# Kernel tuning notes

Hardware: AMD Instinct MI355X
Metric: run time of the kernel (lower is better)

Reference implementation:

```python
import math
import jax, jax.numpy as jnp
import numpy as np
from jax import lax

B, T, D_HEAD, M_FEAT = 8, 8192, 64, 256
EPS = 1e-6


def _draw_omega(key, d, m):
    # Orthogonal random features: QR blocks of size d x d, rows rescaled by
    # the Frobenius row-norms of the original Gaussian blocks (chi scaling).
    n_blocks = math.ceil(m / d)
    blocks = []
    for i in range(n_blocks):
        g = jax.random.normal(jax.random.fold_in(key, i), (d, d), dtype=jnp.float32)
        qb, _ = jnp.linalg.qr(g)
        norms = jnp.linalg.norm(g, axis=1)
        blocks.append(qb * norms[:, None])
    return jnp.concatenate(blocks, axis=0)[:m]


def setup_inputs() -> dict:
    key = jax.random.key(0)
    kq, kk, kv, ko = jax.random.split(key, 4)
    q = jax.random.normal(kq, (B, T, D_HEAD), dtype=jnp.float32)
    k = jax.random.normal(kk, (B, T, D_HEAD), dtype=jnp.float32)
    v = jax.random.normal(kv, (B, T, D_HEAD), dtype=jnp.float32)
    omega = _draw_omega(ko, D_HEAD, M_FEAT)
    return {"q": q, "k": k, "v": v, "omega": omega}


def _positive_map(x, omega):
    # phi(x) = exp(x @ omega^T - ||x||^2/2 - rowmax) / sqrt(m)
    log_phi = x @ omega.T - 0.5 * jnp.sum(x * x, axis=-1, keepdims=True)
    log_phi = log_phi - jnp.max(log_phi, axis=-1, keepdims=True)
    m = omega.shape[0]
    return jnp.exp(log_phi) / jnp.sqrt(jnp.asarray(m, dtype=x.dtype))


def reference(q, k, v, omega):
    scale = 1.0 / math.sqrt(q.shape[-1])
    phi_q = _positive_map(q * scale, omega)  # (B, T, m)
    phi_k = _positive_map(k * scale, omega)  # (B, T, m)

    def step(carry, xs):
        S, z = carry                     # S: (B, m, d), z: (B, m)
        pq, pk, vt = xs                  # each (B, m) / (B, m) / (B, d)
        S = S + pk[:, :, None] * vt[:, None, :]
        z = z + pk
        out = jnp.einsum('bm,bmd->bd', pq, S)
        denom = jnp.sum(pq * z, axis=-1, keepdims=True) + EPS
        return (S, z), out / denom

    S0 = jnp.zeros((q.shape[0], omega.shape[0], v.shape[-1]), dtype=q.dtype)
    z0 = jnp.zeros((q.shape[0], omega.shape[0]), dtype=q.dtype)
    xs = (jnp.swapaxes(phi_q, 0, 1), jnp.swapaxes(phi_k, 0, 1), jnp.swapaxes(v, 0, 1))
    _, outs = lax.scan(step, (S0, z0), xs)   # outs: (T, B, d)
    return jnp.swapaxes(outs, 0, 1)          # (B, T, d)
```

## Files before the change

### kernel.cpp

```cpp
#include <hip/hip_runtime.h>
#include <hip/hip_bf16.h>

typedef __hip_bfloat16 bf16;
typedef __attribute__((ext_vector_type(8))) short short8;
typedef __attribute__((ext_vector_type(4))) short shortx4;
typedef __attribute__((ext_vector_type(4))) float floatx4;

#define NEED_WS_BYTES 110625024ULL

__device__ __forceinline__ float b2f(bf16 x) { return __bfloat162float(x); }
__device__ __forceinline__ bf16  f2b(float x) { return __float2bfloat16(x); }
__device__ __forceinline__ float bflo(unsigned u) { return __uint_as_float(u << 16); }
__device__ __forceinline__ float bfhi(unsigned u) { return __uint_as_float(u & 0xffff0000u); }

__device__ __forceinline__ float ldin(const void* p, size_t i, int isf32) {
  return isf32 ? ((const float*)p)[i] : b2f(((const bf16*)p)[i]);
}

__device__ __forceinline__ short sb(float f) {
  bf16 h = f2b(f * 0.125f);
  return *reinterpret_cast<short*>(&h);
}
__device__ __forceinline__ short scale_b(short u) {
  float f = __uint_as_float(((unsigned)(unsigned short)u) << 16) * 0.125f;
  bf16 h = f2b(f);
  return *reinterpret_cast<short*>(&h);
}

__global__ __launch_bounds__(256) void k_detect(const void* __restrict__ q,
                                                int* __restrict__ flag) {
  __shared__ int cnt;
  if (threadIdx.x == 0) cnt = 0;
  __syncthreads();
  const unsigned short* u = (const unsigned short*)q;
  int c = 0;
  for (int e = threadIdx.x; e < 2048; e += 256) {
    unsigned short w = u[2 * e];
    int ex = (w >> 7) & 0xFF;
    if ((w & 0x7FFF) != 0 && (ex < 110 || ex > 140)) c++;
  }
  atomicAdd(&cnt, c);
  __syncthreads();
  if (threadIdx.x == 0) *flag = (cnt > 512) ? 1 : 0;
}

__global__ __launch_bounds__(256) void k_omega(const void* __restrict__ omega,
                                               bf16* __restrict__ omb,
                                               const int* __restrict__ flag) {
  int isf32 = *flag;
  int e = blockIdx.x * 256 + threadIdx.x;
  omb[e] = f2b(ldin(omega, e, isf32));
}

__device__ __forceinline__ void phi_load_a(const void* src, size_t row, int quad,
                                           int isf32, short8& a0, short8& a1) {
  if (isf32) {
    const float* xr = (const float*)src + row * 64;
    float4 f0 = *reinterpret_cast<const float4*>(xr + quad * 8);
    float4 f1 = *reinterpret_cast<const float4*>(xr + quad * 8 + 4);
    float4 f2 = *reinterpret_cast<const float4*>(xr + 32 + quad * 8);
    float4 f3 = *reinterpret_cast<const float4*>(xr + 32 + quad * 8 + 4);
    a0[0] = sb(f0.x); a0[1] = sb(f0.y); a0[2] = sb(f0.z); a0[3] = sb(f0.w);
    a0[4] = sb(f1.x); a0[5] = sb(f1.y); a0[6] = sb(f1.z); a0[7] = sb(f1.w);
    a1[0] = sb(f2.x); a1[1] = sb(f2.y); a1[2] = sb(f2.z); a1[3] = sb(f2.w);
    a1[4] = sb(f3.x); a1[5] = sb(f3.y); a1[6] = sb(f3.z); a1[7] = sb(f3.w);
  } else {
    const short* xr = (const short*)src + row * 64;
    short8 r0 = *reinterpret_cast<const short8*>(xr + quad * 8);
    short8 r1 = *reinterpret_cast<const short8*>(xr + 32 + quad * 8);
    #pragma unroll
    for (int j = 0; j < 8; ++j) { a0[j] = scale_b(r0[j]); a1[j] = scale_b(r1[j]); }
  }
}

__device__ __forceinline__ void phi_mfma(const bf16* omb, int li, int quad,
                                         const short8& a0, const short8& a1,
                                         floatx4* c, float* mx) {
  #pragma unroll
  for (int n0 = 0; n0 < 16; ++n0) {
    const short* bp = (const short*)omb + (size_t)(n0 * 16 + li) * 64 + quad * 8;
    short8 b0 = *reinterpret_cast<const short8*>(bp);
    short8 b1 = *reinterpret_cast<const short8*>(bp + 32);
    floatx4 acc = {0.f, 0.f, 0.f, 0.f};
    acc = __builtin_amdgcn_mfma_f32_16x16x32_bf16(a0, b0, acc, 0, 0, 0);
    acc = __builtin_amdgcn_mfma_f32_16x16x32_bf16(a1, b1, acc, 0, 0, 0);
    c[n0] = acc;
  }
  #pragma unroll
  for (int r = 0; r < 4; ++r) {
    float m = c[0][r];
    #pragma unroll
    for (int n0 = 1; n0 < 16; ++n0) m = fmaxf(m, c[n0][r]);
    mx[r] = m;
  }
  #pragma unroll
  for (int mask = 1; mask < 16; mask <<= 1) {
    #pragma unroll
    for (int r = 0; r < 4; ++r) mx[r] = fmaxf(mx[r], __shfl_xor(mx[r], mask, 64));
  }
}

__global__ __launch_bounds__(256)
__attribute__((amdgpu_waves_per_eu(1, 2))) void k_phik(
    const void* __restrict__ k, const void* __restrict__ v,
    const bf16* __restrict__ omb, bf16* __restrict__ phiK,
    bf16* __restrict__ SlocT, float* __restrict__ zloc,
    const int* __restrict__ flag) {
  __shared__ short ob[4][16][136];
  __shared__ short pkT[256 * 72];
  __shared__ short vTh[64 * 72];
  __shared__ short vTl[64 * 72];
  __shared__ float zpart[4][256];

  int isf32 = *flag;
  int tid = threadIdx.x;
  size_t tok0 = (size_t)blockIdx.x * 64;
  int li = tid & 15;
  int quad = (tid >> 4) & 3;
  int w = tid >> 6;
  int m0 = w * 16;
  size_t row = tok0 + m0 + li;

  #pragma unroll
  for (int it = 0; it < 16; ++it) {
    int e = it * 256 + tid;
    int tau = e >> 6, d = e & 63;
    float vv = ldin(v, tok0 * 64 + e, isf32);
    bf16 h = f2b(vv);
    bf16 l = f2b(vv - b2f(h));
    vTh[d * 72 + tau] = *reinterpret_cast<short*>(&h);
    vTl[d * 72 + tau] = *reinterpret_cast<short*>(&l);
  }

  short8 a0, a1;
  phi_load_a(k, row, quad, isf32, a0, a1);
  floatx4 c[16];
  float mx[4];
  phi_mfma(omb, li, quad, a0, a1, c, mx);

  float zl[16];
  #pragma unroll
  for (int f = 0; f < 16; ++f) zl[f] = 0.f;
  size_t srow = tok0 + m0 + li;
  #pragma unroll
  for (int h = 0; h < 2; ++h) {
    #pragma unroll
    for (int r = 0; r < 4; ++r) {
      #pragma unroll
      for (int n = 0; n < 8; ++n) {
        bf16 hv = f2b(__expf(c[h * 8 + n][r] - mx[r]) * 0.0625f);
        short hb = *reinterpret_cast<short*>(&hv);
        ob[w][quad * 4 + r][n * 16 + li] = hb;
        pkT[((h * 8 + n) * 16 + li) * 72 + (m0 + quad * 4 + r)] = hb;
        zl[h * 8 + n] += bflo((unsigned)(unsigned short)hb);
      }
    }
    #pragma unroll
    for (int it = 0; it < 4; ++it) {
      int ch = it * 4 + quad;
      short8 vv = *reinterpret_cast<const short8*>(&ob[w][li][ch * 8]);
      *reinterpret_cast<short8*>((short*)phiK + srow * 256 + h * 128 + ch * 8) = vv;
    }
  }
  #pragma unroll
  for (int f = 0; f < 16; ++f) {
    float vz = zl[f];
    vz += __shfl_xor(vz, 16, 64);
    vz += __shfl_xor(vz, 32, 64);
    if (quad == 0) zpart[w][f * 16 + li] = vz;
  }

  __syncthreads();

  int wbase = w * 64;
  floatx4 sa[4][4];
  #pragma unroll
  for (int mt = 0; mt < 4; ++mt)
    #pragma unroll
    for (int n0 = 0; n0 < 4; ++n0) sa[mt][n0] = (floatx4){0.f, 0.f, 0.f, 0.f};

  #pragma unroll
  for (int h = 0; h < 2; ++h) {
    short8 Ah[4], Al[4];
    #pragma unroll
    for (int mt = 0; mt < 4; ++mt) {
      Ah[mt] = *reinterpret_cast<const short8*>(
          &vTh[(mt * 16 + li) * 72 + h * 32 + quad * 8]);
      Al[mt] = *reinterpret_cast<const short8*>(
          &vTl[(mt * 16 + li) * 72 + h * 32 + quad * 8]);
    }
    #pragma unroll
    for (int n0 = 0; n0 < 4; ++n0) {
      short8 Bq = *reinterpret_cast<const short8*>(
          &pkT[(wbase + n0 * 16 + li) * 72 + h * 32 + quad * 8]);
      #pragma unroll
      for (int mt = 0; mt < 4; ++mt) {
        sa[mt][n0] =
            __builtin_amdgcn_mfma_f32_16x16x32_bf16(Ah[mt], Bq, sa[mt][n0], 0, 0, 0);
        sa[mt][n0] =
            __builtin_amdgcn_mfma_f32_16x16x32_bf16(Al[mt], Bq, sa[mt][n0], 0, 0, 0);
      }
    }
  }

  bf16* Sb = SlocT + (size_t)blockIdx.x * 16384;
  #pragma unroll
  for (int mt = 0; mt < 4; ++mt)
    #pragma unroll
    for (int n0 = 0; n0 < 4; ++n0)
      #pragma unroll
      for (int r = 0; r < 4; ++r)
        Sb[(mt * 16 + quad * 4 + r) * 256 + wbase + n0 * 16 + li] =
            f2b(sa[mt][n0][r]);

  {
    int i2 = tid;
    float zz = zpart[0][i2] + zpart[1][i2] + zpart[2][i2] + zpart[3][i2];
    zloc[(size_t)blockIdx.x * 256 + i2] = zz;
  }
}

__global__ __launch_bounds__(64) void k_sprefix(bf16* __restrict__ SlocT) {
  int b = blockIdx.x >> 7, g = blockIdx.x & 127;
  int p = g * 64 + threadIdx.x;
  unsigned* base = (unsigned*)(SlocT + (size_t)b * 2097152) + p;
  float r0 = 0.f, r1 = 0.f;
  #pragma unroll 1
  for (int g16 = 0; g16 < 8; ++g16) {
    unsigned vb[16];
    #pragma unroll
    for (int j = 0; j < 16; ++j) vb[j] = base[(size_t)(g16 * 16 + j) * 8192];
    #pragma unroll
    for (int j = 0; j < 16; ++j) {
      unsigned u = vb[j];
      float t0 = bflo(u), t1 = bfhi(u);
      bf16 h0 = f2b(r0), h1 = f2b(r1);
      vb[j] = ((unsigned)*(unsigned short*)&h0) |
              (((unsigned)*(unsigned short*)&h1) << 16);
      r0 += t0; r1 += t1;
    }
    #pragma unroll
    for (int j = 0; j < 16; ++j) base[(size_t)(g16 * 16 + j) * 8192] = vb[j];
  }
}

__global__ __launch_bounds__(64) void k_zprefix(float* __restrict__ zloc) {
  int b = blockIdx.x >> 2, ig = blockIdx.x & 3;
  int i = ig * 64 + threadIdx.x;
  float* base = zloc + (size_t)b * 32768 + i;
  float run = 0.f;
  #pragma unroll 1
  for (int g16 = 0; g16 < 8; ++g16) {
    float vb[16];
    #pragma unroll
    for (int j = 0; j < 16; ++j) vb[j] = base[(size_t)(g16 * 16 + j) * 256];
    #pragma unroll
    for (int j = 0; j < 16; ++j) { float t = vb[j]; vb[j] = run; run += t; }
    #pragma unroll
    for (int j = 0; j < 16; ++j) base[(size_t)(g16 * 16 + j) * 256] = vb[j];
  }
}

__global__ __launch_bounds__(256)
__attribute__((amdgpu_waves_per_eu(1, 2))) void k_out(
    const void* __restrict__ q, const bf16* __restrict__ omb,
    const bf16* __restrict__ phiK, const void* __restrict__ v,
    const bf16* __restrict__ SlocT, const float* __restrict__ zloc,
    void* __restrict__ outp, const int* __restrict__ flag) {
  __shared__ short spT[64 * 264];
  __shared__ short vTh[64 * 72];
  __shared__ short vTl[64 * 72];
  __shared__ short aT[64 * 72];

  int isf32 = *flag;
  int chunk = blockIdx.x;
  size_t tok0 = (size_t)chunk * 64;
  int tid = threadIdx.x;
  int lane = tid & 63;
  int li = lane & 15;
  int quad = lane >> 4;
  int w = __builtin_amdgcn_readfirstlane(tid >> 6);
  int m0 = w * 16;

  #pragma unroll
  for (int it = 0; it < 16; ++it) {
    int e = it * 256 + tid;
    int tau = e >> 6, d = e & 63;
    float vv = ldin(v, tok0 * 64 + e, isf32);
    bf16 h = f2b(vv);
    bf16 l = f2b(vv - b2f(h));
    vTh[d * 72 + tau] = *reinterpret_cast<short*>(&h);
    vTl[d * 72 + tau] = *reinterpret_cast<short*>(&l);
  }
  {
    shortx4 z4 = {0, 0, 0, 0};
    int arow0 = m0 + li;
    for (int cc = (w + 1) * 16 + quad * 4; cc < 64; cc += 16)
      *reinterpret_cast<shortx4*>(&aT[arow0 * 72 + cc]) = z4;
  }

  float dpart[4] = {0.f, 0.f, 0.f, 0.f};
  {
    short8 qa0, qa1;
    phi_load_a(q, tok0 + m0 + li, quad, isf32, qa0, qa1);
    floatx4 c[16];
    float mx[4];
    phi_mfma(omb, li, quad, qa0, qa1, c, mx);

    const float* zp = zloc + (size_t)chunk * 256;
    #pragma unroll
    for (int n0 = 0; n0 < 16; ++n0) {
      float zv = zp[n0 * 16 + li];
      #pragma unroll
      for (int r = 0; r < 4; ++r) {
        bf16 hv = f2b(__expf(c[n0][r] - mx[r]) * 0.0625f);
        short hb = *reinterpret_cast<short*>(&hv);
        spT[(m0 + quad * 4 + r) * 264 + n0 * 16 + li] = hb;
        dpart[r] += bflo((unsigned)(unsigned short)hb) * zv;
      }
    }
  }

  const short* pqf = &spT[(m0 + li) * 264 + quad * 8];
  short8 a1[8];
  #pragma unroll
  for (int kk = 0; kk < 8; ++kk)
    a1[kk] = *reinterpret_cast<const short8*>(pqf + kk * 32);

  __syncthreads();

  {
    const short* src = (const short*)SlocT + (size_t)chunk * 16384;
    #pragma unroll
    for (int it = 0; it < 8; ++it) {
      int e = it * 256 + tid;
      int d = e >> 5, seg = e & 31;
      *reinterpret_cast<short8*>(&spT[d * 264 + seg * 8]) =
          *reinterpret_cast<const short8*>(src + d * 256 + seg * 8);
    }
  }

  floatx4 c1[4];
  #pragma unroll
  for (int n0 = 0; n0 < 4; ++n0) c1[n0] = (floatx4){0.f, 0.f, 0.f, 0.f};
  const short* pkb = (const short*)phiK + tok0 * 256;
  #pragma unroll
  for (int n0 = 0; n0 < 4; ++n0) {
    if (n0 <= w) {
      const short* bp = pkb + (size_t)(n0 * 16 + li) * 256 + quad * 8;
      floatx4 acc = c1[n0];
      #pragma unroll
      for (int kk = 0; kk < 8; ++kk) {
        short8 b = *reinterpret_cast<const short8*>(bp + kk * 32);
        acc = __builtin_amdgcn_mfma_f32_16x16x32_bf16(a1[kk], b, acc, 0, 0, 0);
      }
      c1[n0] = acc;
    }
  }

  #pragma unroll
  for (int n0 = 0; n0 < 4; ++n0) {
    if (n0 <= w) {
      int tau = n0 * 16 + li;
      #pragma unroll
      for (int r = 0; r < 4; ++r) {
        int t = m0 + quad * 4 + r;
        float val = (tau <= t) ? c1[n0][r] : 0.f;
        dpart[r] += val;
        bf16 hh = f2b(val);
        aT[t * 72 + tau] = *reinterpret_cast<short*>(&hh);
      }
    }
  }

  __syncthreads();

  floatx4 o[4];
  #pragma unroll
  for (int n0 = 0; n0 < 4; ++n0) o[n0] = (floatx4){0.f, 0.f, 0.f, 0.f};

  const short* arow = &aT[(m0 + li) * 72 + quad * 8];
  short8 a3_0 = *reinterpret_cast<const short8*>(arow);
  short8 a3_1 = *reinterpret_cast<const short8*>(arow + 32);

  #pragma unroll
  for (int n0 = 0; n0 < 4; ++n0) {
    floatx4 acc = o[n0];
    const short* sp = &spT[(n0 * 16 + li) * 264 + quad * 8];
    #pragma unroll
    for (int kk = 0; kk < 8; ++kk) {
      short8 b = *reinterpret_cast<const short8*>(sp + kk * 32);
      acc = __builtin_amdgcn_mfma_f32_16x16x32_bf16(a1[kk], b, acc, 0, 0, 0);
    }
    const short* vph = &vTh[(n0 * 16 + li) * 72 + quad * 8];
    const short* vpl = &vTl[(n0 * 16 + li) * 72 + quad * 8];
    short8 bh0 = *reinterpret_cast<const short8*>(vph);
    short8 bh1 = *reinterpret_cast<const short8*>(vph + 32);
    short8 bl0 = *reinterpret_cast<const short8*>(vpl);
    short8 bl1 = *reinterpret_cast<const short8*>(vpl + 32);
    acc = __builtin_amdgcn_mfma_f32_16x16x32_bf16(a3_0, bh0, acc, 0, 0, 0);
    acc = __builtin_amdgcn_mfma_f32_16x16x32_bf16(a3_1, bh1, acc, 0, 0, 0);
    acc = __builtin_amdgcn_mfma_f32_16x16x32_bf16(a3_0, bl0, acc, 0, 0, 0);
    acc = __builtin_amdgcn_mfma_f32_16x16x32_bf16(a3_1, bl1, acc, 0, 0, 0);
    o[n0] = acc;
  }

  #pragma unroll
  for (int mask = 1; mask < 16; mask <<= 1) {
    #pragma unroll
    for (int r = 0; r < 4; ++r) dpart[r] += __shfl_xor(dpart[r], mask, 64);
  }

  #pragma unroll
  for (int r = 0; r < 4; ++r) {
    float rd = 1.f / (dpart[r] + 1e-6f);
    size_t obb = (tok0 + m0 + quad * 4 + r) * 64 + li;
    if (isf32) {
      float* op = (float*)outp + obb;
      #pragma unroll
      for (int n0 = 0; n0 < 4; ++n0) op[n0 * 16] = o[n0][r] * rd;
    } else {
      bf16* op = (bf16*)outp + obb;
      #pragma unroll
      for (int n0 = 0; n0 < 4; ++n0) op[n0 * 16] = f2b(o[n0][r] * rd);
    }
  }
}

extern "C" void kernel_launch(void* const* d_in, const int* in_sizes, int n_in,
                              void* d_out, int out_size, void* d_ws, size_t ws_size,
                              hipStream_t stream) {
  (void)in_sizes; (void)n_in; (void)out_size;
  if (ws_size < NEED_WS_BYTES) return;

  const void* q = d_in[0];
  const void* k = d_in[1];
  const void* v = d_in[2];
  const void* omega = d_in[3];

  int*   flag = (int*)d_ws;
  float* wsf  = (float*)d_ws + 64;
  bf16*  omb  = (bf16*)wsf;
  float* zloc = wsf + 131072;
  bf16*  Sloc = (bf16*)(wsf + 393216);
  bf16*  phiK = (bf16*)(wsf + 17170432);

  k_detect<<<1, 256, 0, stream>>>(q, flag);
  k_omega<<<64, 256, 0, stream>>>(omega, omb, flag);
  k_phik<<<1024, 256, 0, stream>>>(k, v, omb, phiK, Sloc, zloc, flag);
  k_sprefix<<<1024, 64, 0, stream>>>(Sloc);
  k_zprefix<<<32, 64, 0, stream>>>(zloc);
  k_out<<<1024, 256, 0, stream>>>(q, omb, phiK, v, Sloc, zloc, d_out, flag);
}
```

Baseline: 194.6 us.

## Merge prefix kernels into parallel 4-wave scan and swizzle phiK LDS layout

Replaces the two serial chunk-prefix kernels, each using 64-thread blocks, with one merged kernel. Each block has four waves that each sum a quarter of the chunks and combine their partial totals through shared memory, so the serial dependency chain is shorter and one launch is saved. In k_phik, the padded pkT tile is replaced with an XOR-swizzled 64-wide layout, the ob staging buffer is removed so phiK is written directly with scalar stores, and z is computed from pkT after the barrier. The occupancy hint is raised to 3 waves per EU. The risks are uncoalesced 2-byte global stores for phiK and more register pressure from holding 32 values per thread in the prefix.

```diff
diff --git a/kernel.cpp b/kernel.cpp
--- a/kernel.cpp
+++ b/kernel.cpp
@@ -101,16 +101,14 @@
 }
 
 __global__ __launch_bounds__(256)
-__attribute__((amdgpu_waves_per_eu(1, 2))) void k_phik(
+__attribute__((amdgpu_waves_per_eu(1, 3))) void k_phik(
     const void* __restrict__ k, const void* __restrict__ v,
     const bf16* __restrict__ omb, bf16* __restrict__ phiK,
     bf16* __restrict__ SlocT, float* __restrict__ zloc,
     const int* __restrict__ flag) {
-  __shared__ short ob[4][16][136];
-  __shared__ short pkT[256 * 72];
+  __shared__ short pkT[256 * 64];
   __shared__ short vTh[64 * 72];
   __shared__ short vTl[64 * 72];
-  __shared__ float zpart[4][256];
 
   int isf32 = *flag;
   int tid = threadIdx.x;
@@ -138,39 +136,34 @@
   float mx[4];
   phi_mfma(omb, li, quad, a0, a1, c, mx);
 
-  float zl[16];
-  #pragma unroll
-  for (int f = 0; f < 16; ++f) zl[f] = 0.f;
-  size_t srow = tok0 + m0 + li;
-  #pragma unroll
-  for (int h = 0; h < 2; ++h) {
+  #pragma unroll
+  for (int n0 = 0; n0 < 16; ++n0) {
     #pragma unroll
     for (int r = 0; r < 4; ++r) {
-      #pragma unroll
-      for (int n = 0; n < 8; ++n) {
-        bf16 hv = f2b(__expf(c[h * 8 + n][r] - mx[r]) * 0.0625f);
-        short hb = *reinterpret_cast<short*>(&hv);
-        ob[w][quad * 4 + r][n * 16 + li] = hb;
-        pkT[((h * 8 + n) * 16 + li) * 72 + (m0 + quad * 4 + r)] = hb;
-        zl[h * 8 + n] += bflo((unsigned)(unsigned short)hb);
-      }
-    }
-    #pragma unroll
-    for (int it = 0; it < 4; ++it) {
-      int ch = it * 4 + quad;
-      short8 vv = *reinterpret_cast<const short8*>(&ob[w][li][ch * 8]);
-      *reinterpret_cast<short8*>((short*)phiK + srow * 256 + h * 128 + ch * 8) = vv;
-    }
-  }
-  #pragma unroll
-  for (int f = 0; f < 16; ++f) {
-    float vz = zl[f];
-    vz += __shfl_xor(vz, 16, 64);
-    vz += __shfl_xor(vz, 32, 64);
-    if (quad == 0) zpart[w][f * 16 + li] = vz;
+      bf16 hv = f2b(__expf(c[n0][r] - mx[r]) * 0.0625f);
+      short hb = *reinterpret_cast<short*>(&hv);
+      int i = n0 * 16 + li;
+      int t = m0 + quad * 4 + r;
+      ((short*)phiK)[(tok0 + t) * 256 + i] = hb;
+      int cch = (t >> 3) ^ (i & 7);
+      pkT[i * 64 + cch * 8 + (t & 7)] = hb;
+    }
   }
 
   __syncthreads();
+
+  {
+    int i2 = tid;
+    float zz = 0.f;
+    #pragma unroll
+    for (int c8 = 0; c8 < 8; ++c8) {
+      short8 vv8 = *reinterpret_cast<const short8*>(
+          &pkT[i2 * 64 + (c8 ^ (i2 & 7)) * 8]);
+      #pragma unroll
+      for (int j = 0; j < 8; ++j) zz += bflo((unsigned)(unsigned short)vv8[j]);
+    }
+    zloc[(size_t)blockIdx.x * 256 + i2] = zz;
+  }
 
   int wbase = w * 64;
   floatx4 sa[4][4];
@@ -191,8 +184,9 @@
     }
     #pragma unroll
     for (int n0 = 0; n0 < 4; ++n0) {
-      short8 Bq = *reinterpret_cast<const short8*>(
-          &pkT[(wbase + n0 * 16 + li) * 72 + h * 32 + quad * 8]);
+      int crow = wbase + n0 * 16 + li;
+      int cc = (h * 4 + quad) ^ (li & 7);
+      short8 Bq = *reinterpret_cast<const short8*>(&pkT[crow * 64 + cc * 8]);
       #pragma unroll
       for (int mt = 0; mt < 4; ++mt) {
         sa[mt][n0] =
@@ -212,52 +206,60 @@
       for (int r = 0; r < 4; ++r)
         Sb[(mt * 16 + quad * 4 + r) * 256 + wbase + n0 * 16 + li] =
             f2b(sa[mt][n0][r]);
-
-  {
-    int i2 = tid;
-    float zz = zpart[0][i2] + zpart[1][i2] + zpart[2][i2] + zpart[3][i2];
-    zloc[(size_t)blockIdx.x * 256 + i2] = zz;
-  }
-}
-
-__global__ __launch_bounds__(64) void k_sprefix(bf16* __restrict__ SlocT) {
-  int b = blockIdx.x >> 7, g = blockIdx.x & 127;
-  int p = g * 64 + threadIdx.x;
-  unsigned* base = (unsigned*)(SlocT + (size_t)b * 2097152) + p;
-  float r0 = 0.f, r1 = 0.f;
-  #pragma unroll 1
-  for (int g16 = 0; g16 < 8; ++g16) {
-    unsigned vb[16];
-    #pragma unroll
-    for (int j = 0; j < 16; ++j) vb[j] = base[(size_t)(g16 * 16 + j) * 8192];
-    #pragma unroll
-    for (int j = 0; j < 16; ++j) {
+}
+
+__global__ __launch_bounds__(256) void k_prefix(bf16* __restrict__ SlocT,
+                                                float* __restrict__ zloc) {
+  __shared__ float tot[4][64][2];
+  int tid = threadIdx.x;
+  int lane = tid & 63;
+  int w = tid >> 6;
+  if (blockIdx.x < 1024) {
+    int b = blockIdx.x >> 7, g = blockIdx.x & 127;
+    int p = g * 64 + lane;
+    unsigned* base = (unsigned*)(SlocT + (size_t)b * 2097152) + p;
+    unsigned vb[32];
+    #pragma unroll
+    for (int j = 0; j < 32; ++j) vb[j] = base[(size_t)(w * 32 + j) * 8192];
+    float t0 = 0.f, t1 = 0.f;
+    #pragma unroll
+    for (int j = 0; j < 32; ++j) { t0 += bflo(vb[j]); t1 += bfhi(vb[j]); }
+    tot[w][lane][0] = t0; tot[w][lane][1] = t1;
+    __syncthreads();
+    float r0 = 0.f, r1 = 0.f;
+    for (int w2 = 0; w2 < w; ++w2) {
+      r0 += tot[w2][lane][0]; r1 += tot[w2][lane][1];
+    }
+    #pragma unroll
+    for (int j = 0; j < 32; ++j) {
       unsigned u = vb[j];
-      float t0 = bflo(u), t1 = bfhi(u);
       bf16 h0 = f2b(r0), h1 = f2b(r1);
-      vb[j] = ((unsigned)*(unsigned short*)&h0) |
-              (((unsigned)*(unsigned short*)&h1) << 16);
-      r0 += t0; r1 += t1;
-    }
-    #pragma unroll
-    for (int j = 0; j < 16; ++j) base[(size_t)(g16 * 16 + j) * 8192] = vb[j];
-  }
-}
-
-__global__ __launch_bounds__(64) void k_zprefix(float* __restrict__ zloc) {
-  int b = blockIdx.x >> 2, ig = blockIdx.x & 3;
-  int i = ig * 64 + threadIdx.x;
-  float* base = zloc + (size_t)b * 32768 + i;
-  float run = 0.f;
-  #pragma unroll 1
-  for (int g16 = 0; g16 < 8; ++g16) {
-    float vb[16];
-    #pragma unroll
-    for (int j = 0; j < 16; ++j) vb[j] = base[(size_t)(g16 * 16 + j) * 256];
-    #pragma unroll
-    for (int j = 0; j < 16; ++j) { float t = vb[j]; vb[j] = run; run += t; }
-    #pragma unroll
-    for (int j = 0; j < 16; ++j) base[(size_t)(g16 * 16 + j) * 256] = vb[j];
+      unsigned pw = ((unsigned)*(unsigned short*)&h0) |
+                    (((unsigned)*(unsigned short*)&h1) << 16);
+      base[(size_t)(w * 32 + j) * 8192] = pw;
+      r0 += bflo(u); r1 += bfhi(u);
+    }
+  } else {
+    int idx = blockIdx.x - 1024;
+    int b = idx >> 2, ig = idx & 3;
+    int i = ig * 64 + lane;
+    float* base = zloc + (size_t)b * 32768 + i;
+    float vb[32];
+    #pragma unroll
+    for (int j = 0; j < 32; ++j) vb[j] = base[(size_t)(w * 32 + j) * 256];
+    float t = 0.f;
+    #pragma unroll
+    for (int j = 0; j < 32; ++j) t += vb[j];
+    tot[w][lane][0] = t;
+    __syncthreads();
+    float r = 0.f;
+    for (int w2 = 0; w2 < w; ++w2) r += tot[w2][lane][0];
+    #pragma unroll
+    for (int j = 0; j < 32; ++j) {
+      float tt = vb[j];
+      base[(size_t)(w * 32 + j) * 256] = r;
+      r += tt;
+    }
   }
 }
 
@@ -448,7 +450,6 @@
   k_detect<<<1, 256, 0, stream>>>(q, flag);
   k_omega<<<64, 256, 0, stream>>>(omega, omb, flag);
   k_phik<<<1024, 256, 0, stream>>>(k, v, omb, phiK, Sloc, zloc, flag);
-  k_sprefix<<<1024, 64, 0, stream>>>(Sloc);
-  k_zprefix<<<32, 64, 0, stream>>>(zloc);
+  k_prefix<<<1056, 256, 0, stream>>>(Sloc, zloc);
   k_out<<<1024, 256, 0, stream>>>(q, omb, phiK, v, Sloc, zloc, d_out, flag);
 }
```

Measured after the change: 190.9 us. Within noise of the previous version (-1.9%).
